# Optimization experiments

Hardware: AMD Instinct MI355X
Metric: run time of the kernel (lower is better)

The kernel has to match this reference:

```python
import jax, jax.numpy as jnp
import numpy as np

IMG, P, S, E, B = 224, 16, 8, 128, 64
N = (IMG - P) // S + 1          # patches per spatial dim (27)
L = N * N                       # num patches (729)
K = P * P                       # patch area (256)


def _flat_patch_idx():
    # flattened pixel index for each (patch, within-patch) element, shape [L, K]
    base = jnp.arange(N) * S            # top-left corner of each patch row/col
    off = jnp.arange(P)
    rows = base[:, None] + off[None, :]  # [N, P]
    hh = rows[:, None, :, None]          # [N,1,P,1]
    ww = rows[None, :, None, :]          # [1,N,1,P]
    return (hh * IMG + ww).reshape(L, K)  # row-major over patch positions, i*P+j within patch (matches torch Unfold)


def setup_inputs() -> dict:
    key = jax.random.key(0)
    k = jax.random.split(key, 5)
    x = jax.random.normal(k[0], (B, 3, IMG, IMG), dtype=jnp.float32)
    W_enc = jax.random.normal(k[1], (3, E, K), dtype=jnp.float32) * 0.02
    b_enc = jax.random.normal(k[2], (3, E), dtype=jnp.float32) * 0.02
    W_dec = jax.random.normal(k[3], (3, K, E), dtype=jnp.float32) * 0.02
    b_dec = jax.random.normal(k[4], (3, K), dtype=jnp.float32) * 0.02
    return {"x": x, "W_enc": W_enc, "b_enc": b_enc, "W_dec": W_dec, "b_dec": b_dec}


def reference(x, W_enc, b_enc, W_dec, b_dec):
    flat = _flat_patch_idx()                         # [L, K] int indices, static
    Bn = x.shape[0]
    # unfold: gather overlapping patches -> [B, 3, L, K]
    patches = x.reshape(Bn, 3, IMG * IMG)[:, :, flat]
    # per-channel linear encode: [B,3,L,E]
    emb = jnp.einsum('bclk,cek->bcle', patches, W_enc) + b_enc[:, None, :]
    # per-channel linear decode: [B,3,L,K]
    rec = jnp.einsum('bcle,cke->bclk', emb, W_dec) + b_dec[:, None, :]
    # fold: overlap-add scatter back to image
    fi = flat.reshape(-1)
    out = jnp.zeros((Bn, 3, IMG * IMG), x.dtype).at[:, :, fi].add(rec.reshape(Bn, 3, L * K))
    # normalization = fold(unfold(ones)) = per-pixel overlap count
    count = jnp.zeros((IMG * IMG,), x.dtype).at[fi].add(jnp.ones((L * K,), x.dtype))
    return (out / count).reshape(Bn, 3, IMG, IMG)
```

## Files before the change

kernel.cpp:

```cpp
#include <hip/hip_runtime.h>

#define IMG   224
#define IMG2  (IMG*IMG)
#define NN    27
#define KK    256
#define EE    128
#define SCOLS 232
#define RSTR  136

typedef float f32x4 __attribute__((ext_vector_type(4)));
typedef short s16x8 __attribute__((ext_vector_type(8)));

__device__ __forceinline__ unsigned short f2bf(float f) {
    unsigned int u = __float_as_uint(f);
    u = (u + 0x7fffu + ((u >> 16) & 1u)) >> 16;
    return (unsigned short)u;
}
__device__ __forceinline__ float bf2f(unsigned short u) {
    return __uint_as_float((unsigned int)u << 16);
}
__device__ __forceinline__ uint2 pack4(f32x4 r) {
    uint2 u;
    asm("v_cvt_pk_bf16_f32 %0, %1, %2" : "=v"(u.x) : "v"(r.x), "v"(r.y));
    asm("v_cvt_pk_bf16_f32 %0, %1, %2" : "=v"(u.y) : "v"(r.z), "v"(r.w));
    return u;
}

__global__ void pack_M(const float* __restrict__ W_enc, const float* __restrict__ W_dec,
                       const float* __restrict__ b_enc, const float* __restrict__ b_dec,
                       unsigned short* __restrict__ APK, float* __restrict__ v) {
    int k = blockIdx.x, c = blockIdx.y, j = threadIdx.x;
    const float* wd = W_dec + ((size_t)c*KK + k)*EE;
    const float* we = W_enc + (size_t)c*EE*KK + j;
    float acc = 0.f;
    #pragma unroll 8
    for (int e = 0; e < EE; ++e) acc = fmaf(wd[e], we[(size_t)e*KK], acc);
    int kf = k >> 4, kr = k & 15, jb = j >> 5, g = (j >> 3) & 3, i = j & 7;
    APK[(size_t)c*65536 + (((kf*8 + jb)*64) + g*16 + kr)*8 + i] = f2bf(acc);

    __shared__ float pv[128];
    if (j < EE) pv[j] = wd[j] * b_enc[c*EE + j];
    __syncthreads();
    for (int off = 64; off > 0; off >>= 1) {
        if (j < off) pv[j] += pv[j + off];
        __syncthreads();
    }
    if (j == 0) v[c*KK + k] = pv[0] + b_dec[c*KK + k];
}

__global__ __launch_bounds__(256, 2)
void patch_ae_loop(const float* __restrict__ x, const unsigned short* __restrict__ APK,
                   const float* __restrict__ v, float* __restrict__ out) {
    const int hid = blockIdx.x;
    const int lid = (hid & 7)*96 + (hid >> 3);
    const int q   = lid & 3;
    const int t2  = lid >> 2;
    const int c   = t2 % 3;
    const int b   = t2 / 3;
    const int s0  = 7*q;

    const int tid  = threadIdx.x;
    const int lane = tid & 63, wave = tid >> 6;

    __shared__ __align__(16) unsigned short ring[32*SCOLS];
    __shared__ __align__(16) unsigned short rec[2][30][RSTR];
    __shared__ __align__(16) float vsh[256];

    vsh[tid] = v[c*256 + tid];
    if (tid < RSTR) {
        rec[0][0][tid] = 0; rec[0][28][tid] = 0;
        rec[1][0][tid] = 0; rec[1][28][tid] = 0;
    }

    const int prow   = wave >> 1;
    const int kq     = wave & 1;
    const int kfbase = prow*8 + kq*4;
    const int g = lane >> 4, lr = lane & 15;
    const int jx0 = (g & 1)*8;
    const int c1 = (lr <= 10) ? (128 + 8*lr) : 208;
    const int rowoff = prow ? -8 : 0;

    const int kfu = __builtin_amdgcn_readfirstlane(kfbase);
    const char* abase = (const char*)(APK + (size_t)c*65536) + (size_t)kfu*8192;
    const int vf0 = lane*16,        vf0b = vf0 + 4096;
    const int vf1 = vf0 + 8192,     vf1b = vf1 + 4096;
    const int vf2 = vf0 + 16384,    vf2b = vf2 + 4096;
    const int vf3 = vf0 + 24576,    vf3b = vf3 + 4096;

#define ALD(VAR, VOFF, OFFSTR)                                      \
    asm volatile("global_load_dwordx4 %0, %1, %2 offset:" OFFSTR    \
                 : "=v"(VAR) : "v"(VOFF), "s"(abase));

    s16x8 a0_0,a0_1,a0_2,a0_3,a0_4,a0_5,a0_6,a0_7;
    s16x8 a1_0,a1_1,a1_2,a1_3,a1_4,a1_5,a1_6,a1_7;
    s16x8 a2_0,a2_1,a2_2,a2_3,a2_4,a2_5,a2_6,a2_7;
    s16x8 a3_0,a3_1,a3_2,a3_3,a3_4,a3_5,a3_6,a3_7;
    ALD(a0_0, vf0,  "0")    ALD(a0_1, vf0,  "1024") ALD(a0_2, vf0,  "2048") ALD(a0_3, vf0,  "3072")
    ALD(a0_4, vf0b, "0")    ALD(a0_5, vf0b, "1024") ALD(a0_6, vf0b, "2048") ALD(a0_7, vf0b, "3072")
    ALD(a1_0, vf1,  "0")    ALD(a1_1, vf1,  "1024") ALD(a1_2, vf1,  "2048") ALD(a1_3, vf1,  "3072")
    ALD(a1_4, vf1b, "0")    ALD(a1_5, vf1b, "1024") ALD(a1_6, vf1b, "2048") ALD(a1_7, vf1b, "3072")
    ALD(a2_0, vf2,  "0")    ALD(a2_1, vf2,  "1024") ALD(a2_2, vf2,  "2048") ALD(a2_3, vf2,  "3072")
    ALD(a2_4, vf2b, "0")    ALD(a2_5, vf2b, "1024") ALD(a2_6, vf2b, "2048") ALD(a2_7, vf2b, "3072")
    ALD(a3_0, vf3,  "0")    ALD(a3_1, vf3,  "1024") ALD(a3_2, vf3,  "2048") ALD(a3_3, vf3,  "3072")
    ALD(a3_4, vf3b, "0")    ALD(a3_5, vf3b, "1024") ALD(a3_6, vf3b, "2048") ALD(a3_7, vf3b, "3072")
#undef ALD

    const float* xb = x + (size_t)(b*3 + c)*IMG2;

    #pragma unroll
    for (int it = 0; it < 3; ++it) {
        int ci = tid + it*256;
        if (ci < 672) {
            int r  = ci / 28, cc = ci - (ci/28)*28;
            int ar = 8*s0 - 8 + r;
            int yr = ar < 0 ? 0 : (ar > 223 ? 223 : ar);
            const float4* src = (const float4*)(xb + (size_t)yr*IMG + cc*8);
            float4 lo = src[0], hi = src[1];
            uint2 u0 = pack4((f32x4){lo.x, lo.y, lo.z, lo.w});
            uint2 u1 = pack4((f32x4){hi.x, hi.y, hi.z, hi.w});
            *((uint4*)&ring[(ar & 31)*SCOLS + cc*8]) = make_uint4(u0.x, u0.y, u1.x, u1.y);
        }
    }
    __syncthreads();
    asm volatile("s_waitcnt vmcnt(0)");
    __builtin_amdgcn_sched_barrier(0);

    const int rr  = tid / 28;
    const int cc2 = tid - 28*(tid/28);

    const int eq  = tid % 28, ery = tid / 28;
    const int ev1 = (eq < 27), ev0 = (eq > 0);
    const int ero = ery*16;

#define MFMA2(AF, B0, B1, F)                                                             \
        acc[F][0] = __builtin_amdgcn_mfma_f32_16x16x32_bf16(AF, B0, acc[F][0], 0, 0, 0); \
        acc[F][1] = __builtin_amdgcn_mfma_f32_16x16x32_bf16(AF, B1, acc[F][1], 0, 0, 0);

#define MSTEP(JB, A0, A1, A2, A3)                                                    \
        {                                                                            \
            const int jy = 2*(JB) + (g >> 1);                                        \
            const unsigned short* srow = &ring[((rowb + jy) & 31)*SCOLS + jx0];      \
            s16x8 bf0 = *((const s16x8*)&srow[8*lr]);                                \
            s16x8 bf1 = *((const s16x8*)&srow[c1]);                                  \
            __builtin_amdgcn_s_setprio(1);                                           \
            MFMA2(A0, bf0, bf1, 0) MFMA2(A1, bf0, bf1, 1)                            \
            MFMA2(A2, bf0, bf1, 2) MFMA2(A3, bf0, bf1, 3)                            \
            __builtin_amdgcn_s_setprio(0);                                           \
        }

    #pragma unroll 1
    for (int s = s0; s < s0 + 7; ++s) {
        f32x4 ga0, ga1;
        if (tid < 224) {
            int yr = 8*(s+2) + rr; if (yr > 223) yr = 223;
            int voffx = yr*(IMG*4) + cc2*32;
            asm volatile("global_load_dwordx4 %0, %1, %2"           : "=v"(ga0) : "v"(voffx), "s"(xb));
            asm volatile("global_load_dwordx4 %0, %1, %2 offset:16" : "=v"(ga1) : "v"(voffx), "s"(xb));
        }

        f32x4 acc[4][2];
        #pragma unroll
        for (int f = 0; f < 4; ++f)
            #pragma unroll
            for (int pf = 0; pf < 2; ++pf)
                acc[f][pf] = (f32x4){0.f, 0.f, 0.f, 0.f};
        const int rowb = 8*s + rowoff;
        MSTEP(0, a0_0, a1_0, a2_0, a3_0)
        MSTEP(1, a0_1, a1_1, a2_1, a3_1)
        MSTEP(2, a0_2, a1_2, a2_2, a3_2)
        MSTEP(3, a0_3, a1_3, a2_3, a3_3)
        MSTEP(4, a0_4, a1_4, a2_4, a3_4)
        MSTEP(5, a0_5, a1_5, a2_5, a3_5)
        MSTEP(6, a0_6, a1_6, a2_6, a3_6)
        MSTEP(7, a0_7, a1_7, a2_7, a3_7)

        #pragma unroll
        for (int f = 0; f < 4; ++f) {
            int klocal = kq*64 + f*16 + g*4;
            f32x4 bias = *((const f32x4*)&vsh[prow*128 + klocal]);
            #pragma unroll
            for (int pf = 0; pf < 2; ++pf) {
                f32x4 r = acc[f][pf] + bias;
                int pidx = pf*16 + lr + 1;
                if (pidx >= 28) pidx = 29;
                *((uint2*)&rec[prow][pidx][klocal]) = pack4(r);
            }
        }
        __syncthreads();

        if (tid < 224) {
            asm volatile("s_waitcnt vmcnt(0)");
            __builtin_amdgcn_sched_barrier(0);
            uint2 u0 = pack4(ga0);
            uint2 u1 = pack4(ga1);
            int ar2 = 8*(s+2) + rr;
            *((uint4*)&ring[(ar2 & 31)*SCOLS + cc2*8]) = make_uint4(u0.x, u0.y, u1.x, u1.y);
        }

        if (tid < 224) {
            const int h0 = (s < 27);
            const int h1 = (s > 0);
            const int shift = (ev0 & ev1) + (h0 & h1);
            const float inv = __int_as_float(0x3f800000 - (shift << 23));
            float sum[8];
            #pragma unroll
            for (int d = 0; d < 8; ++d) sum[d] = 0.f;
            if (h0) {
                s16x8 rrv = *((const s16x8*)&rec[0][eq+1][ero]);
                s16x8 llv = *((const s16x8*)&rec[0][eq][ero + 8]);
                #pragma unroll
                for (int d = 0; d < 8; ++d)
                    sum[d] += bf2f((unsigned short)rrv[d]) + bf2f((unsigned short)llv[d]);
            }
            if (h1) {
                s16x8 rrv = *((const s16x8*)&rec[1][eq+1][ero]);
                s16x8 llv = *((const s16x8*)&rec[1][eq][ero + 8]);
                #pragma unroll
                for (int d = 0; d < 8; ++d)
                    sum[d] += bf2f((unsigned short)rrv[d]) + bf2f((unsigned short)llv[d]);
            }
            float* orow = out + (size_t)(b*3 + c)*IMG2 + (size_t)(8*s + ery)*IMG + 8*eq;
            f32x4 o0 = {sum[0]*inv, sum[1]*inv, sum[2]*inv, sum[3]*inv};
            f32x4 o1 = {sum[4]*inv, sum[5]*inv, sum[6]*inv, sum[7]*inv};
            *((f32x4*)orow)       = o0;
            *((f32x4*)(orow + 4)) = o1;
        }
        __syncthreads();
    }
#undef MSTEP
#undef MFMA2
}

extern "C" void kernel_launch(void* const* d_in, const int* in_sizes, int n_in,
                              void* d_out, int out_size, void* d_ws, size_t ws_size,
                              hipStream_t stream) {
    (void)in_sizes; (void)n_in; (void)out_size; (void)ws_size;
    const float* x     = (const float*)d_in[0];
    const float* W_enc = (const float*)d_in[1];
    const float* b_enc = (const float*)d_in[2];
    const float* W_dec = (const float*)d_in[3];
    const float* b_dec = (const float*)d_in[4];
    float* out = (float*)d_out;

    float*          v   = (float*)d_ws;
    unsigned short* APK = (unsigned short*)((char*)d_ws + 4096);

    pack_M<<<dim3(KK, 3), 256, 0, stream>>>(W_enc, W_dec, b_enc, b_dec, APK, v);
    patch_ae_loop<<<dim3(768), 256, 0, stream>>>(x, APK, v, out);
}
```

Baseline: 42.36 us.

## Split patch kernel work across eight waves with 512-thread blocks

Doubles the block size to 512 threads so each wave handles two k-fragments instead of four. This halves the per-wave A-operand registers and accumulators, and spreads the MFMA work across more waves. The aim is more latency hiding and occupancy. The trade-off is more waves contending for the shared ring reads and barriers, and the epilogue's thread-count assumptions must still hold.

```diff
diff --git a/kernel.cpp b/kernel.cpp
--- a/kernel.cpp
+++ b/kernel.cpp
@@ -48,7 +48,7 @@
     if (j == 0) v[c*KK + k] = pv[0] + b_dec[c*KK + k];
 }
 
-__global__ __launch_bounds__(256, 2)
+__global__ __launch_bounds__(512, 4)
 void patch_ae_loop(const float* __restrict__ x, const unsigned short* __restrict__ APK,
                    const float* __restrict__ v, float* __restrict__ out) {
     const int hid = blockIdx.x;
@@ -66,15 +66,15 @@
     __shared__ __align__(16) unsigned short rec[2][30][RSTR];
     __shared__ __align__(16) float vsh[256];
 
-    vsh[tid] = v[c*256 + tid];
+    if (tid < 256) vsh[tid] = v[c*256 + tid];
     if (tid < RSTR) {
         rec[0][0][tid] = 0; rec[0][28][tid] = 0;
         rec[1][0][tid] = 0; rec[1][28][tid] = 0;
     }
 
-    const int prow   = wave >> 1;
-    const int kq     = wave & 1;
-    const int kfbase = prow*8 + kq*4;
+    const int prow   = wave >> 2;
+    const int kq     = wave & 3;
+    const int kfbase = prow*8 + kq*2;
     const int g = lane >> 4, lr = lane & 15;
     const int jx0 = (g & 1)*8;
     const int c1 = (lr <= 10) ? (128 + 8*lr) : 208;
@@ -82,10 +82,8 @@
 
     const int kfu = __builtin_amdgcn_readfirstlane(kfbase);
     const char* abase = (const char*)(APK + (size_t)c*65536) + (size_t)kfu*8192;
-    const int vf0 = lane*16,        vf0b = vf0 + 4096;
-    const int vf1 = vf0 + 8192,     vf1b = vf1 + 4096;
-    const int vf2 = vf0 + 16384,    vf2b = vf2 + 4096;
-    const int vf3 = vf0 + 24576,    vf3b = vf3 + 4096;
+    const int v0a = lane*16,       v0b = v0a + 4096;
+    const int v1a = v0a + 8192,    v1b = v0a + 12288;
 
 #define ALD(VAR, VOFF, OFFSTR)                                      \
     asm volatile("global_load_dwordx4 %0, %1, %2 offset:" OFFSTR    \
@@ -93,23 +91,17 @@
 
     s16x8 a0_0,a0_1,a0_2,a0_3,a0_4,a0_5,a0_6,a0_7;
     s16x8 a1_0,a1_1,a1_2,a1_3,a1_4,a1_5,a1_6,a1_7;
-    s16x8 a2_0,a2_1,a2_2,a2_3,a2_4,a2_5,a2_6,a2_7;
-    s16x8 a3_0,a3_1,a3_2,a3_3,a3_4,a3_5,a3_6,a3_7;
-    ALD(a0_0, vf0,  "0")    ALD(a0_1, vf0,  "1024") ALD(a0_2, vf0,  "2048") ALD(a0_3, vf0,  "3072")
-    ALD(a0_4, vf0b, "0")    ALD(a0_5, vf0b, "1024") ALD(a0_6, vf0b, "2048") ALD(a0_7, vf0b, "3072")
-    ALD(a1_0, vf1,  "0")    ALD(a1_1, vf1,  "1024") ALD(a1_2, vf1,  "2048") ALD(a1_3, vf1,  "3072")
-    ALD(a1_4, vf1b, "0")    ALD(a1_5, vf1b, "1024") ALD(a1_6, vf1b, "2048") ALD(a1_7, vf1b, "3072")
-    ALD(a2_0, vf2,  "0")    ALD(a2_1, vf2,  "1024") ALD(a2_2, vf2,  "2048") ALD(a2_3, vf2,  "3072")
-    ALD(a2_4, vf2b, "0")    ALD(a2_5, vf2b, "1024") ALD(a2_6, vf2b, "2048") ALD(a2_7, vf2b, "3072")
-    ALD(a3_0, vf3,  "0")    ALD(a3_1, vf3,  "1024") ALD(a3_2, vf3,  "2048") ALD(a3_3, vf3,  "3072")
-    ALD(a3_4, vf3b, "0")    ALD(a3_5, vf3b, "1024") ALD(a3_6, vf3b, "2048") ALD(a3_7, vf3b, "3072")
+    ALD(a0_0, v0a, "0")  ALD(a0_1, v0a, "1024") ALD(a0_2, v0a, "2048") ALD(a0_3, v0a, "3072")
+    ALD(a0_4, v0b, "0")  ALD(a0_5, v0b, "1024") ALD(a0_6, v0b, "2048") ALD(a0_7, v0b, "3072")
+    ALD(a1_0, v1a, "0")  ALD(a1_1, v1a, "1024") ALD(a1_2, v1a, "2048") ALD(a1_3, v1a, "3072")
+    ALD(a1_4, v1b, "0")  ALD(a1_5, v1b, "1024") ALD(a1_6, v1b, "2048") ALD(a1_7, v1b, "3072")
 #undef ALD
 
     const float* xb = x + (size_t)(b*3 + c)*IMG2;
 
     #pragma unroll
-    for (int it = 0; it < 3; ++it) {
-        int ci = tid + it*256;
+    for (int it = 0; it < 2; ++it) {
+        int ci = tid + it*512;
         if (ci < 672) {
             int r  = ci / 28, cc = ci - (ci/28)*28;
             int ar = 8*s0 - 8 + r;
@@ -136,7 +128,7 @@
         acc[F][0] = __builtin_amdgcn_mfma_f32_16x16x32_bf16(AF, B0, acc[F][0], 0, 0, 0); \
         acc[F][1] = __builtin_amdgcn_mfma_f32_16x16x32_bf16(AF, B1, acc[F][1], 0, 0, 0);
 
-#define MSTEP(JB, A0, A1, A2, A3)                                                    \
+#define MSTEP(JB, A0, A1)                                                            \
         {                                                                            \
             const int jy = 2*(JB) + (g >> 1);                                        \
             const unsigned short* srow = &ring[((rowb + jy) & 31)*SCOLS + jx0];      \
@@ -144,7 +136,6 @@
             s16x8 bf1 = *((const s16x8*)&srow[c1]);                                  \
             __builtin_amdgcn_s_setprio(1);                                           \
             MFMA2(A0, bf0, bf1, 0) MFMA2(A1, bf0, bf1, 1)                            \
-            MFMA2(A2, bf0, bf1, 2) MFMA2(A3, bf0, bf1, 3)                            \
             __builtin_amdgcn_s_setprio(0);                                           \
         }
 
@@ -158,25 +149,25 @@
             asm volatile("global_load_dwordx4 %0, %1, %2 offset:16" : "=v"(ga1) : "v"(voffx), "s"(xb));
         }
 
-        f32x4 acc[4][2];
+        f32x4 acc[2][2];
         #pragma unroll
-        for (int f = 0; f < 4; ++f)
+        for (int f = 0; f < 2; ++f)
             #pragma unroll
             for (int pf = 0; pf < 2; ++pf)
                 acc[f][pf] = (f32x4){0.f, 0.f, 0.f, 0.f};
         const int rowb = 8*s + rowoff;
-        MSTEP(0, a0_0, a1_0, a2_0, a3_0)
-        MSTEP(1, a0_1, a1_1, a2_1, a3_1)
-        MSTEP(2, a0_2, a1_2, a2_2, a3_2)
-        MSTEP(3, a0_3, a1_3, a2_3, a3_3)
-        MSTEP(4, a0_4, a1_4, a2_4, a3_4)
-        MSTEP(5, a0_5, a1_5, a2_5, a3_5)
-        MSTEP(6, a0_6, a1_6, a2_6, a3_6)
-        MSTEP(7, a0_7, a1_7, a2_7, a3_7)
+        MSTEP(0, a0_0, a1_0)
+        MSTEP(1, a0_1, a1_1)
+        MSTEP(2, a0_2, a1_2)
+        MSTEP(3, a0_3, a1_3)
+        MSTEP(4, a0_4, a1_4)
+        MSTEP(5, a0_5, a1_5)
+        MSTEP(6, a0_6, a1_6)
+        MSTEP(7, a0_7, a1_7)
 
         #pragma unroll
-        for (int f = 0; f < 4; ++f) {
-            int klocal = kq*64 + f*16 + g*4;
+        for (int f = 0; f < 2; ++f) {
+            int klocal = kq*32 + f*16 + g*4;
             f32x4 bias = *((const f32x4*)&vsh[prow*128 + klocal]);
             #pragma unroll
             for (int pf = 0; pf < 2; ++pf) {
@@ -246,5 +237,5 @@
     unsigned short* APK = (unsigned short*)((char*)d_ws + 4096);
 
     pack_M<<<dim3(KK, 3), 256, 0, stream>>>(W_enc, W_dec, b_enc, b_dec, APK, v);
-    patch_ae_loop<<<dim3(768), 256, 0, stream>>>(x, APK, v, out);
-}
+    patch_ae_loop<<<dim3(768), 512, 0, stream>>>(x, APK, v, out);
+}
```

After: 41.01 us. 1.03x faster.
